# Kernel tuning notes

Measured on AMD Instinct MI355X. Metric: run time of the kernel, lower is better.

## Reference

```python
import jax, jax.numpy as jnp
import numpy as np

# Tsit5 (Tsitouras 2011) explicit RK tableau coefficients (5th-order solution weights)
A21 = 0.161
A31, A32 = -0.008480655492356989, 0.335480655492357
A41, A42, A43 = 2.8971530571054935, -6.359448489975075, 4.3622954328695815
A51, A52, A53, A54 = 5.325864828439257, -11.748883564062828, 7.4955393428898365, -0.09249506636175525
A61, A62, A63, A64, A65 = 5.86145544294642, -12.92096931784711, 8.159367898576159, -0.071584973281401, -0.028269050394068383
B1, B2, B3, B4, B5, B6 = 0.09646076681806523, 0.01, 0.4798896504144996, 1.379008574103742, -3.290069515436081, 2.324710524099774

BATCH, D, H, T = 4096, 64, 256, 128


def net_apply(y, W1, b1, W2, b2):
    # y: [B, D] -> dy/dt: [B, D]  (MLP vector field, autonomous)
    return jnp.tanh(y @ W1 + b1) @ W2 + b2


def tsit5_step(f, y, h):
    # One explicit Tsit5 step of size h on state y: [B, D]
    k1 = f(y)
    k2 = f(y + h * (A21 * k1))
    k3 = f(y + h * (A31 * k1 + A32 * k2))
    k4 = f(y + h * (A41 * k1 + A42 * k2 + A43 * k3))
    k5 = f(y + h * (A51 * k1 + A52 * k2 + A53 * k3 + A54 * k4))
    k6 = f(y + h * (A61 * k1 + A62 * k2 + A63 * k3 + A64 * k4 + A65 * k5))
    return y + h * (B1 * k1 + B2 * k2 + B3 * k3 + B4 * k4 + B5 * k5 + B6 * k6)


def setup_inputs() -> dict:
    key = jax.random.key(0)
    k0, k1, k2 = jax.random.split(key, 3)
    y0 = jax.random.normal(k0, (BATCH, D), dtype=jnp.float32)
    ts = jnp.arange(T, dtype=jnp.float32) * 0.05  # save times
    W1 = jax.random.normal(k1, (D, H), dtype=jnp.float32) / np.sqrt(D)
    b1 = jnp.zeros((H,), dtype=jnp.float32)
    W2 = jax.random.normal(k2, (H, D), dtype=jnp.float32) / np.sqrt(H)
    b2 = jnp.zeros((D,), dtype=jnp.float32)
    return {"y0": y0, "ts": ts, "W1": W1, "b1": b1, "W2": W2, "b2": b2, "n_sub": 8}


def reference(y0, ts, W1, b1, W2, b2, n_sub):
    # Integrate dy/dt = net(y) with fixed-step Tsit5 (n_sub substeps per save interval),
    # returning the trajectory at save points ts: [B, T, D].
    f = lambda y: net_apply(y, W1, b1, W2, b2)

    def interval(y, dt):
        h = dt / n_sub
        def sub(yc, _):
            return tsit5_step(f, yc, h), None
        y, _ = jax.lax.scan(sub, y, None, length=n_sub)
        return y, y

    dts = jnp.diff(ts)                      # [T-1]
    _, ys = jax.lax.scan(interval, y0, dts)  # [T-1, B, D]
    traj = jnp.concatenate([y0[None], ys], axis=0)  # [T, B, D]
    return jnp.transpose(traj, (1, 0, 2))   # [B, T, D]
```

## Files before the change

kernel.cpp:

```cpp
#include <hip/hip_runtime.h>
#include <hip/hip_bf16.h>

typedef __bf16 bf16x8 __attribute__((ext_vector_type(8)));
typedef float f32x4 __attribute__((ext_vector_type(4)));

#define MFMA_B16(a,b,c) __builtin_amdgcn_mfma_f32_16x16x32_bf16((a),(b),(c),0,0,0)

#define A21f 0.161f
#define A31f (-0.008480655492356989f)
#define A32f 0.335480655492357f
#define A41f 2.8971530571054935f
#define A42f (-6.359448489975075f)
#define A43f 4.3622954328695815f
#define A51f 5.325864828439257f
#define A52f (-11.748883564062828f)
#define A53f 7.4955393428898365f
#define A54f (-0.09249506636175525f)
#define A61f 5.86145544294642f
#define A62f (-12.92096931784711f)
#define A63f 8.159367898576159f
#define A64f (-0.071584973281401f)
#define A65f (-0.028269050394068383f)
#define B1f 0.09646076681806523f
#define B2f 0.01f
#define B3f 0.4798896504144996f
#define B4f 1.379008574103742f
#define B5f (-3.290069515436081f)
#define B6f 2.324710524099774f

constexpr int T_SAVE = 128;
constexpr int DIM = 64;
constexpr int HID = 256;

__device__ __forceinline__ float fast_exp2(float x){
#if __has_builtin(__builtin_amdgcn_exp2f)
  return __builtin_amdgcn_exp2f(x);
#else
  return exp2f(x);
#endif
}
__device__ __forceinline__ float fast_rcp(float x){
#if __has_builtin(__builtin_amdgcn_rcpf)
  return __builtin_amdgcn_rcpf(x);
#else
  return 1.0f / x;
#endif
}
__device__ __forceinline__ float tanh_fast(float x){
  float t = fast_exp2(x * 2.8853900817779268f);
  return 1.0f - 2.0f * fast_rcp(t + 1.0f);
}
__device__ __forceinline__ f32x4 splat4(float x){ return f32x4{x,x,x,x}; }

__global__ __launch_bounds__(512, 2)
void node_tsit5_kernel(const float* __restrict__ y0, const float* __restrict__ ts,
                       const float* __restrict__ W1g, const float* __restrict__ b1g,
                       const float* __restrict__ W2g, const float* __restrict__ b2g,
                       const int* __restrict__ nsub_p, float* __restrict__ out)
{
  const int tid = (int)threadIdx.x;
  const int w   = tid >> 6;
  const int l   = tid & 63;
  const int c   = l & 15;
  const int g   = l >> 4;
  const int wq  = w & 3;
  const bool hiW = (w < 4);
  const int rowbase = (int)blockIdx.x * 16;

  __shared__ __align__(16) __bf16 Yh[2*64*8];
  __shared__ __align__(16) __bf16 Yl[2*64*8];
  __shared__ __align__(16) __bf16 Hh[8*64*8];
  __shared__ __align__(16) __bf16 Hl[8*64*8];
  __shared__ float ts_s[T_SAVE];

  if (tid < T_SAVE) ts_s[tid] = ts[tid];

  const int nsub = nsub_p[0];

  bf16x8 w1h[2][2], w1l[2][2];
#pragma unroll
  for (int nt = 0; nt < 2; ++nt) {
    const int col = (2*w + nt)*16 + c;
#pragma unroll
    for (int ks = 0; ks < 2; ++ks)
#pragma unroll
      for (int j = 0; j < 8; ++j) {
        float v = W1g[(ks*32 + g*8 + j)*HID + col];
        __bf16 hi = (__bf16)v;
        w1h[nt][ks][j] = hi;
        w1l[nt][ks][j] = (__bf16)(v - (float)hi);
      }
  }
  bf16x8 w2h[8], w2l[8];
#pragma unroll
  for (int ks = 0; ks < 8; ++ks)
#pragma unroll
    for (int j = 0; j < 8; ++j) {
      float v = W2g[(ks*32 + g*8 + j)*DIM + (wq*16 + c)];
      __bf16 hi = (__bf16)v;
      w2h[ks][j] = hi;
      w2l[ks][j] = (__bf16)(v - (float)hi);
    }
  float b1v[2];
#pragma unroll
  for (int nt = 0; nt < 2; ++nt) b1v[nt] = b1g[(2*w + nt)*16 + c];
  const float b2v = b2g[wq*16 + c];

  const int d_    = wq*16 + c;
  const int physL = l ^ ((l >> 3) & 3);

  int yoff[4];
#pragma unroll
  for (int s = 0; s < 4; ++s) {
    int row = 4*g + s;
    int lp  = row | (((d_ >> 3) & 3) << 4);
    int ph  = lp ^ ((lp >> 3) & 3);
    yoff[s] = (d_ >> 5)*512 + ph*8 + (d_ & 7);
  }
  int hoff[2][4];
#pragma unroll
  for (int nt = 0; nt < 2; ++nt) {
    int jcol = (2*w + nt)*16 + c;
#pragma unroll
    for (int r = 0; r < 4; ++r) {
      int row = 4*g + r;
      int lp  = row | (((jcol >> 3) & 3) << 4);
      int ph  = lp ^ ((lp >> 3) & 3);
      hoff[nt][r] = (jcol >> 5)*512 + ph*8 + (jcol & 7);
    }
  }

  f32x4 y4;
#pragma unroll
  for (int s = 0; s < 4; ++s) {
    int row = rowbase + 4*g + s;
    y4[s] = y0[row*DIM + d_];
    if (hiW) out[(size_t)row*(T_SAVE*DIM) + d_] = y4[s];
  }
  __syncthreads();

  f32x4 ysv = y4;

  auto feval = [&]() -> f32x4 {
    if (hiW) {
#pragma unroll
      for (int s = 0; s < 4; ++s) Yh[yoff[s]] = (__bf16)ysv[s];
    } else {
#pragma unroll
      for (int s = 0; s < 4; ++s) {
        float hi = (float)(__bf16)ysv[s];
        Yl[yoff[s]] = (__bf16)(ysv[s] - hi);
      }
    }
    __syncthreads();
    bf16x8 ah0 = *(const bf16x8*)&Yh[physL*8];
    bf16x8 ah1 = *(const bf16x8*)&Yh[512 + physL*8];
    bf16x8 al0 = *(const bf16x8*)&Yl[physL*8];
    bf16x8 al1 = *(const bf16x8*)&Yl[512 + physL*8];
    f32x4 p0 = {0.f,0.f,0.f,0.f}, q0 = {0.f,0.f,0.f,0.f};
    f32x4 p1 = {0.f,0.f,0.f,0.f}, q1 = {0.f,0.f,0.f,0.f};
    p0 = MFMA_B16(ah0, w1h[0][0], p0);  q0 = MFMA_B16(ah1, w1h[0][1], q0);
    p1 = MFMA_B16(ah0, w1h[1][0], p1);  q1 = MFMA_B16(ah1, w1h[1][1], q1);
    p0 = MFMA_B16(ah0, w1l[0][0], p0);  q0 = MFMA_B16(ah1, w1l[0][1], q0);
    p1 = MFMA_B16(ah0, w1l[1][0], p1);  q1 = MFMA_B16(ah1, w1l[1][1], q1);
    p0 = MFMA_B16(al0, w1h[0][0], p0);  q0 = MFMA_B16(al1, w1h[0][1], q0);
    p1 = MFMA_B16(al0, w1h[1][0], p1);  q1 = MFMA_B16(al1, w1h[1][1], q1);
    f32x4 h0 = p0 + q0, h1 = p1 + q1;
#pragma unroll
    for (int r = 0; r < 4; ++r) {
      float th = tanh_fast(h0[r] + b1v[0]);
      __bf16 hi = (__bf16)th;
      Hh[hoff[0][r]] = hi;
      Hl[hoff[0][r]] = (__bf16)(th - (float)hi);
    }
#pragma unroll
    for (int r = 0; r < 4; ++r) {
      float th = tanh_fast(h1[r] + b1v[1]);
      __bf16 hi = (__bf16)th;
      Hh[hoff[1][r]] = hi;
      Hl[hoff[1][r]] = (__bf16)(th - (float)hi);
    }
    __syncthreads();
    f32x4 aA = {0.f,0.f,0.f,0.f}, aB = {0.f,0.f,0.f,0.f}, aC = {0.f,0.f,0.f,0.f};
#pragma unroll
    for (int ks = 0; ks < 8; ++ks) {
      bf16x8 ah = *(const bf16x8*)&Hh[ks*512 + physL*8];
      bf16x8 al = *(const bf16x8*)&Hl[ks*512 + physL*8];
      aA = MFMA_B16(ah, w2h[ks], aA);
      aB = MFMA_B16(ah, w2l[ks], aB);
      aC = MFMA_B16(al, w2h[ks], aC);
    }
    return (aA + aB) + aC + splat4(b2v);
  };

  for (int iv = 0; iv < T_SAVE-1; ++iv) {
    const float h = (ts_s[iv+1] - ts_s[iv]) / (float)nsub;
    const f32x4 h4 = splat4(h);
    for (int sub = 0; sub < nsub; ++sub) {
      f32x4 k1 = feval();
      ysv = y4 + h4 * (splat4(A21f) * k1);
      f32x4 k2 = feval();
      {
        f32x4 t = splat4(A31f)*k1 + splat4(A32f)*k2;
        ysv = y4 + h4 * t;
      }
      f32x4 k3 = feval();
      {
        f32x4 t = splat4(A41f)*k1 + splat4(A42f)*k2 + splat4(A43f)*k3;
        ysv = y4 + h4 * t;
      }
      f32x4 k4 = feval();
      {
        f32x4 t = splat4(A51f)*k1 + splat4(A52f)*k2 + splat4(A53f)*k3
                + splat4(A54f)*k4;
        ysv = y4 + h4 * t;
      }
      f32x4 k5 = feval();
      {
        f32x4 t = splat4(A61f)*k1 + splat4(A62f)*k2 + splat4(A63f)*k3
                + splat4(A64f)*k4 + splat4(A65f)*k5;
        ysv = y4 + h4 * t;
      }
      f32x4 k6 = feval();
      {
        f32x4 t = splat4(B1f)*k1 + splat4(B2f)*k2 + splat4(B3f)*k3
                + splat4(B4f)*k4 + splat4(B5f)*k5 + splat4(B6f)*k6;
        y4 = y4 + h4 * t;
        ysv = y4;
      }
    }
    if (hiW) {
#pragma unroll
      for (int s = 0; s < 4; ++s) {
        int row = rowbase + 4*g + s;
        out[(size_t)row*(T_SAVE*DIM) + (size_t)(iv+1)*DIM + d_] = y4[s];
      }
    }
  }
}

extern "C" void kernel_launch(void* const* d_in, const int* in_sizes, int n_in,
                              void* d_out, int out_size, void* d_ws, size_t ws_size,
                              hipStream_t stream) {
  const float* y0 = (const float*)d_in[0];
  const float* ts = (const float*)d_in[1];
  const float* W1 = (const float*)d_in[2];
  const float* b1 = (const float*)d_in[3];
  const float* W2 = (const float*)d_in[4];
  const float* b2 = (const float*)d_in[5];
  const int* nsub = (const int*)d_in[6];
  float* out = (float*)d_out;

  const int Bnum = in_sizes[0] / DIM;
  const int nblocks = Bnum / 16;
  node_tsit5_kernel<<<nblocks, 512, 0, stream>>>(y0, ts, W1, b1, W2, b2, nsub, out);
}
```

Baseline: 7.351 ms.

## Split second GEMM over K across wave halves and pack hi/lo bf16 in LDS

Before, every wave held all 8 K-slices of W2 and the two halves of the workgroup computed the same output tiles. Now each half of the workgroup handles half of the hidden dimension, and the partial results are reduced through an LDS exchange buffer. This halves the W2 register footprint and the redundant MFMA work. The hi/lo bf16 split is now packed into a single u32 per element in LDS and unpacked with perm instructions, so one store replaces separate Yh/Yl and Hh/Hl writes. In exchange it adds a third barrier per function evaluation plus an extra LDS round trip for the reduction.

```diff
diff --git a/kernel.cpp b/kernel.cpp
--- a/kernel.cpp
+++ b/kernel.cpp
@@ -3,6 +3,8 @@
 
 typedef __bf16 bf16x8 __attribute__((ext_vector_type(8)));
 typedef float f32x4 __attribute__((ext_vector_type(4)));
+typedef unsigned int u32;
+typedef u32 u32x4 __attribute__((ext_vector_type(4)));
 
 #define MFMA_B16(a,b,c) __builtin_amdgcn_mfma_f32_16x16x32_bf16((a),(b),(c),0,0,0)
 
@@ -52,6 +54,24 @@
 }
 __device__ __forceinline__ f32x4 splat4(float x){ return f32x4{x,x,x,x}; }
 
+__device__ __forceinline__ u32 pack_hl(float x){
+  u32 xu = __float_as_uint(x);
+  float lo = x - __uint_as_float(xu & 0xFFFF0000u);
+  __bf16 lb = (__bf16)lo;
+  unsigned short ls; __builtin_memcpy(&ls, &lb, 2);
+  return ((u32)ls << 16) | (xu >> 16);
+}
+
+__device__ __forceinline__ void unpack_hl(const u32* p, bf16x8& ah, bf16x8& al){
+  union { u32 d[4]; bf16x8 v; } H, L;
+#pragma unroll
+  for (int j = 0; j < 4; ++j) {
+    H.d[j] = __builtin_amdgcn_perm(p[2*j+1], p[2*j], 0x05040100u);
+    L.d[j] = __builtin_amdgcn_perm(p[2*j+1], p[2*j], 0x07060302u);
+  }
+  ah = H.v; al = L.v;
+}
+
 __global__ __launch_bounds__(512, 2)
 void node_tsit5_kernel(const float* __restrict__ y0, const float* __restrict__ ts,
                        const float* __restrict__ W1g, const float* __restrict__ b1g,
@@ -63,14 +83,14 @@
   const int l   = tid & 63;
   const int c   = l & 15;
   const int g   = l >> 4;
-  const int wq  = w & 3;
-  const bool hiW = (w < 4);
+  const bool state = (w < 4);
+  const int tile = state ? w : (w - 4);
+  const int kh   = state ? 0 : 1;
   const int rowbase = (int)blockIdx.x * 16;
 
-  __shared__ __align__(16) __bf16 Yh[2*64*8];
-  __shared__ __align__(16) __bf16 Yl[2*64*8];
-  __shared__ __align__(16) __bf16 Hh[8*64*8];
-  __shared__ __align__(16) __bf16 Hl[8*64*8];
+  __shared__ __align__(16) u32 Yp[1024];
+  __shared__ __align__(16) u32 Hp[4096];
+  __shared__ __align__(16) f32x4 Pex[256];
   __shared__ float ts_s[T_SAVE];
 
   if (tid < T_SAVE) ts_s[tid] = ts[tid];
@@ -82,115 +102,114 @@
   for (int nt = 0; nt < 2; ++nt) {
     const int col = (2*w + nt)*16 + c;
 #pragma unroll
-    for (int ks = 0; ks < 2; ++ks)
+    for (int s = 0; s < 2; ++s)
 #pragma unroll
       for (int j = 0; j < 8; ++j) {
-        float v = W1g[(ks*32 + g*8 + j)*HID + col];
+        float v = W1g[(s*32 + g*8 + j)*HID + col];
         __bf16 hi = (__bf16)v;
-        w1h[nt][ks][j] = hi;
-        w1l[nt][ks][j] = (__bf16)(v - (float)hi);
-      }
-  }
-  bf16x8 w2h[8], w2l[8];
-#pragma unroll
-  for (int ks = 0; ks < 8; ++ks)
+        w1h[nt][s][j] = hi;
+        w1l[nt][s][j] = (__bf16)(v - (float)hi);
+      }
+  }
+  bf16x8 w2h[4], w2l[4];
+#pragma unroll
+  for (int i = 0; i < 4; ++i) {
+    const int ks = 4*kh + i;
 #pragma unroll
     for (int j = 0; j < 8; ++j) {
-      float v = W2g[(ks*32 + g*8 + j)*DIM + (wq*16 + c)];
+      float v = W2g[(ks*32 + g*8 + j)*DIM + (tile*16 + c)];
       __bf16 hi = (__bf16)v;
-      w2h[ks][j] = hi;
-      w2l[ks][j] = (__bf16)(v - (float)hi);
-    }
+      w2h[i][j] = hi;
+      w2l[i][j] = (__bf16)(v - (float)hi);
+    }
+  }
   float b1v[2];
 #pragma unroll
   for (int nt = 0; nt < 2; ++nt) b1v[nt] = b1g[(2*w + nt)*16 + c];
-  const float b2v = b2g[wq*16 + c];
-
-  const int d_    = wq*16 + c;
-  const int physL = l ^ ((l >> 3) & 3);
-
-  int yoff[4];
-#pragma unroll
-  for (int s = 0; s < 4; ++s) {
-    int row = 4*g + s;
-    int lp  = row | (((d_ >> 3) & 3) << 4);
-    int ph  = lp ^ ((lp >> 3) & 3);
-    yoff[s] = (d_ >> 5)*512 + ph*8 + (d_ & 7);
-  }
-  int hoff[2][4];
-#pragma unroll
-  for (int nt = 0; nt < 2; ++nt) {
-    int jcol = (2*w + nt)*16 + c;
-#pragma unroll
-    for (int r = 0; r < 4; ++r) {
-      int row = 4*g + r;
-      int lp  = row | (((jcol >> 3) & 3) << 4);
-      int ph  = lp ^ ((lp >> 3) & 3);
-      hoff[nt][r] = (jcol >> 5)*512 + ph*8 + (jcol & 7);
-    }
-  }
-
-  f32x4 y4;
-#pragma unroll
-  for (int s = 0; s < 4; ++s) {
-    int row = rowbase + 4*g + s;
-    y4[s] = y0[row*DIM + d_];
-    if (hiW) out[(size_t)row*(T_SAVE*DIM) + d_] = y4[s];
+  const float b2v = b2g[tile*16 + c];
+
+  const int rdDw = (l ^ ((l >> 2) & 3)) * 8;
+
+  int hoffDw[2][4];
+#pragma unroll
+  for (int nt = 0; nt < 2; ++nt)
+#pragma unroll
+    for (int r = 0; r < 4; ++r)
+      hoffDw[nt][r] = w*512 + (nt*2 + (c>>3))*128 + 32*g + 8*(r ^ g) + (c & 7);
+  int yoffDw[4];
+#pragma unroll
+  for (int s = 0; s < 4; ++s)
+    yoffDw[s] = (w>>1)*512 + ((w&1)*2 + (c>>3))*128 + 32*g + 8*(s ^ g) + (c & 7);
+
+  const int d_ = tile*16 + c;
+  f32x4 y4 = {0.f,0.f,0.f,0.f};
+  if (state) {
+#pragma unroll
+    for (int s = 0; s < 4; ++s) {
+      int row = rowbase + 4*g + s;
+      y4[s] = y0[row*DIM + d_];
+      out[(size_t)row*(T_SAVE*DIM) + d_] = y4[s];
+    }
   }
   __syncthreads();
 
   f32x4 ysv = y4;
 
   auto feval = [&]() -> f32x4 {
-    if (hiW) {
-#pragma unroll
-      for (int s = 0; s < 4; ++s) Yh[yoff[s]] = (__bf16)ysv[s];
-    } else {
-#pragma unroll
-      for (int s = 0; s < 4; ++s) {
-        float hi = (float)(__bf16)ysv[s];
-        Yl[yoff[s]] = (__bf16)(ysv[s] - hi);
-      }
+    if (state) {
+#pragma unroll
+      for (int s = 0; s < 4; ++s) Yp[yoffDw[s]] = pack_hl(ysv[s]);
     }
     __syncthreads();
-    bf16x8 ah0 = *(const bf16x8*)&Yh[physL*8];
-    bf16x8 ah1 = *(const bf16x8*)&Yh[512 + physL*8];
-    bf16x8 al0 = *(const bf16x8*)&Yl[physL*8];
-    bf16x8 al1 = *(const bf16x8*)&Yl[512 + physL*8];
-    f32x4 p0 = {0.f,0.f,0.f,0.f}, q0 = {0.f,0.f,0.f,0.f};
-    f32x4 p1 = {0.f,0.f,0.f,0.f}, q1 = {0.f,0.f,0.f,0.f};
-    p0 = MFMA_B16(ah0, w1h[0][0], p0);  q0 = MFMA_B16(ah1, w1h[0][1], q0);
-    p1 = MFMA_B16(ah0, w1h[1][0], p1);  q1 = MFMA_B16(ah1, w1h[1][1], q1);
-    p0 = MFMA_B16(ah0, w1l[0][0], p0);  q0 = MFMA_B16(ah1, w1l[0][1], q0);
-    p1 = MFMA_B16(ah0, w1l[1][0], p1);  q1 = MFMA_B16(ah1, w1l[1][1], q1);
-    p0 = MFMA_B16(al0, w1h[0][0], p0);  q0 = MFMA_B16(al1, w1h[0][1], q0);
-    p1 = MFMA_B16(al0, w1h[1][0], p1);  q1 = MFMA_B16(al1, w1h[1][1], q1);
-    f32x4 h0 = p0 + q0, h1 = p1 + q1;
-#pragma unroll
-    for (int r = 0; r < 4; ++r) {
-      float th = tanh_fast(h0[r] + b1v[0]);
-      __bf16 hi = (__bf16)th;
-      Hh[hoff[0][r]] = hi;
-      Hl[hoff[0][r]] = (__bf16)(th - (float)hi);
-    }
-#pragma unroll
-    for (int r = 0; r < 4; ++r) {
-      float th = tanh_fast(h1[r] + b1v[1]);
-      __bf16 hi = (__bf16)th;
-      Hh[hoff[1][r]] = hi;
-      Hl[hoff[1][r]] = (__bf16)(th - (float)hi);
-    }
+    u32 py[8], pz[8];
+    *(u32x4*)&py[0] = *(const u32x4*)&Yp[rdDw];
+    *(u32x4*)&py[4] = *(const u32x4*)&Yp[rdDw + 4];
+    *(u32x4*)&pz[0] = *(const u32x4*)&Yp[512 + rdDw];
+    *(u32x4*)&pz[4] = *(const u32x4*)&Yp[512 + rdDw + 4];
+    bf16x8 ah0, al0, ah1, al1;
+    unpack_hl(py, ah0, al0);
+    unpack_hl(pz, ah1, al1);
+    f32x4 t0a={0.f,0.f,0.f,0.f}, t0b={0.f,0.f,0.f,0.f};
+    f32x4 t1a={0.f,0.f,0.f,0.f}, t1b={0.f,0.f,0.f,0.f};
+    t0a = MFMA_B16(ah0, w1h[0][0], t0a);  t0b = MFMA_B16(ah1, w1h[0][1], t0b);
+    t1a = MFMA_B16(ah0, w1h[1][0], t1a);  t1b = MFMA_B16(ah1, w1h[1][1], t1b);
+    t0a = MFMA_B16(ah0, w1l[0][0], t0a);  t0b = MFMA_B16(ah1, w1l[0][1], t0b);
+    t1a = MFMA_B16(ah0, w1l[1][0], t1a);  t1b = MFMA_B16(ah1, w1l[1][1], t1b);
+    t0a = MFMA_B16(al0, w1h[0][0], t0a);  t0b = MFMA_B16(al1, w1h[0][1], t0b);
+    t1a = MFMA_B16(al0, w1h[1][0], t1a);  t1b = MFMA_B16(al1, w1h[1][1], t1b);
+    f32x4 ht0 = t0a + t0b, ht1 = t1a + t1b;
+#pragma unroll
+    for (int r = 0; r < 4; ++r)
+      Hp[hoffDw[0][r]] = pack_hl(tanh_fast(ht0[r] + b1v[0]));
+#pragma unroll
+    for (int r = 0; r < 4; ++r)
+      Hp[hoffDw[1][r]] = pack_hl(tanh_fast(ht1[r] + b1v[1]));
     __syncthreads();
-    f32x4 aA = {0.f,0.f,0.f,0.f}, aB = {0.f,0.f,0.f,0.f}, aC = {0.f,0.f,0.f,0.f};
-#pragma unroll
-    for (int ks = 0; ks < 8; ++ks) {
-      bf16x8 ah = *(const bf16x8*)&Hh[ks*512 + physL*8];
-      bf16x8 al = *(const bf16x8*)&Hl[ks*512 + physL*8];
-      aA = MFMA_B16(ah, w2h[ks], aA);
-      aB = MFMA_B16(ah, w2l[ks], aB);
-      aC = MFMA_B16(al, w2h[ks], aC);
-    }
-    return (aA + aB) + aC + splat4(b2v);
+    u32 ph[4][8];
+#pragma unroll
+    for (int i = 0; i < 4; ++i) {
+      const int ks = 4*kh + i;
+      *(u32x4*)&ph[i][0] = *(const u32x4*)&Hp[ks*512 + rdDw];
+      *(u32x4*)&ph[i][4] = *(const u32x4*)&Hp[ks*512 + rdDw + 4];
+    }
+    f32x4 aA={0.f,0.f,0.f,0.f}, aB={0.f,0.f,0.f,0.f}, aC={0.f,0.f,0.f,0.f};
+#pragma unroll
+    for (int i = 0; i < 4; ++i) {
+      bf16x8 ah, al;
+      unpack_hl(ph[i], ah, al);
+      aA = MFMA_B16(ah, w2h[i], aA);
+      aB = MFMA_B16(ah, w2l[i], aB);
+      aC = MFMA_B16(al, w2h[i], aC);
+    }
+    f32x4 part = (aA + aB) + aC;
+    if (!state) Pex[tile*64 + l] = part;
+    __syncthreads();
+    f32x4 kout = {0.f,0.f,0.f,0.f};
+    if (state) {
+      f32x4 q = Pex[tile*64 + l];
+      kout = (part + q) + splat4(b2v);
+    }
+    return kout;
   };
 
   for (int iv = 0; iv < T_SAVE-1; ++iv) {
@@ -198,38 +217,38 @@
     const f32x4 h4 = splat4(h);
     for (int sub = 0; sub < nsub; ++sub) {
       f32x4 k1 = feval();
-      ysv = y4 + h4 * (splat4(A21f) * k1);
+      if (state) ysv = y4 + h4 * (splat4(A21f) * k1);
       f32x4 k2 = feval();
-      {
+      if (state) {
         f32x4 t = splat4(A31f)*k1 + splat4(A32f)*k2;
         ysv = y4 + h4 * t;
       }
       f32x4 k3 = feval();
-      {
+      if (state) {
         f32x4 t = splat4(A41f)*k1 + splat4(A42f)*k2 + splat4(A43f)*k3;
         ysv = y4 + h4 * t;
       }
       f32x4 k4 = feval();
-      {
+      if (state) {
         f32x4 t = splat4(A51f)*k1 + splat4(A52f)*k2 + splat4(A53f)*k3
                 + splat4(A54f)*k4;
         ysv = y4 + h4 * t;
       }
       f32x4 k5 = feval();
-      {
+      if (state) {
         f32x4 t = splat4(A61f)*k1 + splat4(A62f)*k2 + splat4(A63f)*k3
                 + splat4(A64f)*k4 + splat4(A65f)*k5;
         ysv = y4 + h4 * t;
       }
       f32x4 k6 = feval();
-      {
+      if (state) {
         f32x4 t = splat4(B1f)*k1 + splat4(B2f)*k2 + splat4(B3f)*k3
                 + splat4(B4f)*k4 + splat4(B5f)*k5 + splat4(B6f)*k6;
         y4 = y4 + h4 * t;
         ysv = y4;
       }
     }
-    if (hiW) {
+    if (state) {
 #pragma unroll
       for (int s = 0; s < 4; ++s) {
         int row = rowbase + 4*g + s;
```

Result: no change. 7.348 ms (-0.0%).
